# Kernel optimization log

Hardware: AMD Instinct MI355X
Metric: run time of the kernel (lower is better)

Reference implementation:

```python
import jax, jax.numpy as jnp
import numpy as np

EPS = 1e-5

def conv1x1(x, w, b):
    # x: [B,C,H,W], w: [O,C], b: [O]
    return jnp.einsum('bchw,oc->bohw', x, w) + b[None, :, None, None]

def bn(x, gamma, beta, mean, var):
    scale = gamma * jax.lax.rsqrt(var + EPS)
    return x * scale[None, :, None, None] + (beta - mean * scale)[None, :, None, None]

def setup_inputs() -> dict:
    key = jax.random.key(0)
    ks = jax.random.split(key, 20)
    B, C, H, W = 4, 64, 512, 512
    O = C
    d = {'feature': jax.random.normal(ks[0], (B, C, H, W), dtype=jnp.float32)}
    i = 1
    for name in ('q', 'k', 'v'):
        d[f'w_{name}'] = jax.random.normal(ks[i], (O, C), dtype=jnp.float32) * 0.05; i += 1
        d[f'b_{name}'] = jnp.zeros((O,), dtype=jnp.float32)
        d[f'gamma_{name}'] = jnp.ones((O,), dtype=jnp.float32)
        d[f'beta_{name}'] = jnp.zeros((O,), dtype=jnp.float32)
        d[f'mean_{name}'] = jax.random.normal(ks[i], (O,), dtype=jnp.float32) * 0.1; i += 1
        d[f'var_{name}'] = jax.random.uniform(ks[i], (O,), dtype=jnp.float32) + 0.5; i += 1
    d['w_out'] = jax.random.normal(ks[i], (O, O), dtype=jnp.float32) * 0.05; i += 1
    d['b_out'] = jnp.zeros((O,), dtype=jnp.float32)
    d['gamma_out'] = jnp.ones((O,), dtype=jnp.float32)
    d['beta_out'] = jnp.zeros((O,), dtype=jnp.float32)
    d['mean_out'] = jax.random.normal(ks[i], (O,), dtype=jnp.float32) * 0.1; i += 1
    d['var_out'] = jax.random.uniform(ks[i], (O,), dtype=jnp.float32) + 0.5
    return d

def reference(feature,
              w_q, b_q, gamma_q, beta_q, mean_q, var_q,
              w_k, b_k, gamma_k, beta_k, mean_k, var_k,
              w_v, b_v, gamma_v, beta_v, mean_v, var_v,
              w_out, b_out, gamma_out, beta_out, mean_out, var_out):
    # feature: [B,C,H,W]; attention treats H as sequence, W as feature dim per (b,c)
    q = bn(conv1x1(feature, w_q, b_q), gamma_q, beta_q, mean_q, var_q)
    k = bn(conv1x1(feature, w_k, b_k), gamma_k, beta_k, mean_k, var_k)
    v = bn(conv1x1(feature, w_v, b_v), gamma_v, beta_v, mean_v, var_v)
    W = q.shape[-1]
    scale = 1.0 / jnp.sqrt(jnp.float32(W))
    # scores: [B,C,H,H] = q @ k^T over the W axis
    scores = jnp.einsum('bchw,bcgw->bchg', q, k) * scale
    attn = jax.nn.softmax(scores, axis=-1)
    attn_out = jnp.einsum('bchg,bcgw->bchw', attn, v)  # [B,C,H,W]
    out = bn(conv1x1(attn_out, w_out, b_out), gamma_out, beta_out, mean_out, var_out)
    # dropout is identity in eval mode
    return out + feature
```

## Files before the change

### kernel.cpp

```cpp
#include <hip/hip_runtime.h>
#include <math.h>

typedef unsigned short u16;
typedef unsigned int u32;
typedef unsigned long long u64;
typedef __attribute__((ext_vector_type(8))) short bf16x8;
typedef __attribute__((ext_vector_type(4))) float f32x4;

#define MFMA16(a,b,c) __builtin_amdgcn_mfma_f32_16x16x32_bf16(a,b,c,0,0,0)

typedef __attribute__((address_space(1))) const unsigned int as1_u32;
typedef __attribute__((address_space(3))) unsigned int as3_u32;
__device__ __forceinline__ void gld16(const u16* g, u16* l){
  __builtin_amdgcn_global_load_lds((as1_u32*)g, (as3_u32*)l, 16, 0, 0);
}

__device__ __forceinline__ u16 f2bf(float x){
  union { float f; u32 u; } v; v.f = x;
  u32 u = v.u;
  return (u16)((u + 0x7fffu + ((u>>16)&1u)) >> 16);
}

__device__ __forceinline__ void memfence(){ asm volatile("" ::: "memory"); }

union B8 { bf16x8 v; u32 u[4]; uint4 q; };

__global__ void k0_prep(const float* wm, const float* bias, const float* gamma,
                        const float* beta, const float* mean, const float* var,
                        float extra, u16* wdst, float* ddst)
{
  int t = threadIdx.x;
  if (t < 64){
    float a0 = gamma[t] * rsqrtf(var[t] + 1e-5f);
    ddst[t] = (beta[t] + (bias[t] - mean[t]) * a0) * extra;
  }
  for (int i = t; i < 4096; i += 256){
    int o = i >> 6;
    float a0 = gamma[o] * rsqrtf(var[o] + 1e-5f);
    wdst[i] = f2bf(wm[i] * a0 * extra);
  }
}

__global__ __launch_bounds__(256,3)
void k1_qkv(const float* __restrict__ f, const u16* __restrict__ wz,
            const float* __restrict__ dz, u16* __restrict__ q,
            u16* __restrict__ kk_, u16* __restrict__ vt)
{
  int bid = blockIdx.x;
  int b  = bid >> 8;
  int ht = (bid >> 3) & 31;
  int wt = bid & 7;
  int tid = threadIdx.x;
  int wv = tid >> 6, lane = tid & 63;
  int l15 = lane & 15, l4 = lane >> 4;
  int h0 = ht * 16;
  int w0 = wt * 64 + wv * 16;

  bf16x8 wa[3][4][2];
  #pragma unroll
  for (int mt=0; mt<3; mt++)
    #pragma unroll
    for (int m=0;m<4;m++)
      #pragma unroll
      for (int ks=0;ks<2;ks++){
        B8 t; t.q = *(const uint4*)(wz + mt*4096 + (m*16+l15)*64 + ks*32 + l4*8);
        wa[mt][m][ks] = t.v;
      }
  f32x4 dv[3][4];
  #pragma unroll
  for (int mt=0;mt<3;mt++)
    #pragma unroll
    for (int m=0;m<4;m++)
      dv[mt][m] = *(const f32x4*)(dz + mt*64 + m*16 + l4*4);

  __shared__ u16 vstage[4][8704];
  u16* vs = vstage[wv];

  B8 bf[2];
  #pragma unroll
  for (int ks=0;ks<2;ks++)
    #pragma unroll
    for (int jj=0;jj<4;jj++){
      int c0 = ks*32 + l4*8 + jj*2;
      size_t i0 = ((size_t)(b*64 + c0)*512 + h0)*512 + w0 + l15;
      bf[ks].u[jj] = (u32)f2bf(f[i0]) | ((u32)f2bf(f[i0 + 262144]) << 16);
    }

  for (int hh=0; hh<16; hh++){
    int h = h0 + hh;
    B8 bfn[2];
    if (hh < 15){
      #pragma unroll
      for (int ks=0;ks<2;ks++)
        #pragma unroll
        for (int jj=0;jj<4;jj++){
          int c0 = ks*32 + l4*8 + jj*2;
          size_t i0 = ((size_t)(b*64 + c0)*512 + h + 1)*512 + w0 + l15;
          bfn[ks].u[jj] = (u32)f2bf(f[i0]) | ((u32)f2bf(f[i0 + 262144]) << 16);
        }
    }
    #pragma unroll
    for (int mt=0; mt<3; mt++){
      f32x4 acc[4];
      #pragma unroll
      for (int m=0;m<4;m++) acc[m] = (f32x4){0.f,0.f,0.f,0.f};
      #pragma unroll
      for (int m=0;m<4;m++)
        #pragma unroll
        for (int ks=0;ks<2;ks++)
          acc[m] = MFMA16(wa[mt][m][ks], bf[ks].v, acc[m]);
      #pragma unroll
      for (int m=0;m<4;m++)
        #pragma unroll
        for (int r=0;r<4;r++){
          float val = acc[m][r] + dv[mt][m][r];
          u16 bv = f2bf(val);
          int o = m*16 + l4*4 + r;
          if (mt==0)      q  [((size_t)(b*64+o)*512 + h)*512 + w0 + l15] = bv;
          else if (mt==1) kk_[((size_t)(b*64+o)*512 + h)*512 + w0 + l15] = bv;
          else            vs[o*136 + l15*8 + (hh&7)] = bv;
        }
    }
    bf[0] = bfn[0]; bf[1] = bfn[1];
    if ((hh&7)==7){
      __syncthreads();
      int hbg = (h - 7) >> 3;
      #pragma unroll
      for (int rr=0; rr<16; rr++){
        int o = rr*4 + l4;
        uint4 d = *(const uint4*)(vs + o*136 + l15*8);
        *(uint4*)(vt + (size_t)(b*64+o)*262144 + (size_t)hbg*4096
                     + (size_t)(w0+l15)*8) = d;
      }
      __syncthreads();
    }
  }
}

__global__ __launch_bounds__(512,2)
void k23_attn(const u16* __restrict__ q, const u16* __restrict__ kten,
              const u16* __restrict__ vt, u16* __restrict__ o2)
{
  int phys = blockIdx.x;
  int x = phys & 7, j = phys >> 3;
  int qt = j & 3, hh = j >> 2;
  int head = x*32 + hh;
  int q0 = qt*128;
  int b = head >> 6, c = head & 63;

  int tid = threadIdx.x;
  int wv = tid >> 6, lane = tid & 63;
  int l15 = lane & 15, l4 = lane >> 4;

  const u16* qh = q    + (size_t)head*262144;
  const u16* kh = kten + (size_t)head*262144;
  const u16* vh = vt   + (size_t)head*262144;

  __shared__ u16 KB[2][16640];
  __shared__ u16 VB[16384];
  __shared__ u16 Pt[5120];

  auto stageK = [&](int jt, int buf){
    const u16* src = kh + (size_t)jt*16384;
    #pragma unroll
    for (int i=0;i<4;i++){
      int row = i*8 + wv;
      gld16(src + (size_t)row*512 + lane*8, &KB[buf][row*520 + lane*8]);
    }
  };
  auto stageV = [&](int jt){
    const u16* src = vh + (size_t)jt*16384;
    #pragma unroll
    for (int i=0;i<4;i++){
      int slot = i*512 + tid;
      int w = slot >> 2, cc = slot & 3;
      int hbl = (cc - (w>>1)) & 3;
      gld16(src + hbl*4096 + w*8, &VB[slot*8]);
    }
  };

  uint4 qreg[16];
  {
    const u16* qrow = qh + (size_t)(q0 + wv*16 + l15)*512;
    #pragma unroll
    for (int ks=0;ks<16;ks++) qreg[ks] = *(const uint4*)(qrow + ks*32 + l4*8);
  }
  stageK(0, 0); stageV(0); stageK(1, 1);
  asm volatile("s_waitcnt vmcnt(4)" ::: "memory");
  __builtin_amdgcn_s_barrier(); memfence();

  f32x4 oacc[32];
  #pragma unroll
  for (int n=0;n<32;n++) oacc[n] = (f32x4){0.f,0.f,0.f,0.f};
  float m_run[4] = {-1e30f,-1e30f,-1e30f,-1e30f};
  float l_run[4] = {0.f,0.f,0.f,0.f};

  const int kbase = l15*520 + l4*8;
  const int vbase = l15*32  + (((l4 + (l15>>1)) & 3) << 3);
  const int pbase = (wv*16 + l15)*40;
  const int prow  = (wv*16 + l4*4)*40;

  for (int jt=0; jt<16; ++jt){
    int cur = jt & 1;
    const u16* Kc = &KB[cur][0];

    f32x4 sA[2], sB[2];
    #pragma unroll
    for (int n=0;n<2;n++){ sA[n]=(f32x4){0,0,0,0}; sB[n]=(f32x4){0,0,0,0}; }
    __builtin_amdgcn_s_setprio(1);
    #pragma unroll
    for (int ks=0; ks<8; ++ks){
      B8 a; a.q = qreg[ks];
      #pragma unroll
      for (int n=0;n<2;n++){
        B8 bb; bb.q = *(const uint4*)(Kc + kbase + n*8320 + ks*32);
        sA[n] = MFMA16(a.v, bb.v, sA[n]);
      }
    }
    #pragma unroll
    for (int ks=8; ks<16; ++ks){
      B8 a; a.q = qreg[ks];
      #pragma unroll
      for (int n=0;n<2;n++){
        B8 bb; bb.q = *(const uint4*)(Kc + kbase + n*8320 + ks*32);
        sB[n] = MFMA16(a.v, bb.v, sB[n]);
      }
    }
    __builtin_amdgcn_s_setprio(0);
    f32x4 sacc0 = sA[0] + sB[0];
    f32x4 sacc1 = sA[1] + sB[1];

    float pm[4], fc[4];
    bool need = false;
    #pragma unroll
    for (int r=0;r<4;r++){
      float p = fmaxf(sacc0[r], sacc1[r]);
      #pragma unroll
      for (int d=1; d<16; d<<=1) p = fmaxf(p, __shfl_xor(p, d, 64));
      pm[r] = p;
      need = need || (p > m_run[r] + 4.0f);
    }
    if (__any(need ? 1 : 0)){
      #pragma unroll
      for (int r=0;r<4;r++){
        float mn = fmaxf(m_run[r], pm[r]);
        fc[r] = exp2f(m_run[r] - mn);
        m_run[r] = mn;
      }
      #pragma unroll
      for (int n=0;n<32;n++)
        #pragma unroll
        for (int r=0;r<4;r++) oacc[n][r] *= fc[r];
    } else {
      fc[0]=fc[1]=fc[2]=fc[3]=1.0f;
    }
    #pragma unroll
    for (int r=0;r<4;r++){
      float e0 = exp2f(sacc0[r] - m_run[r]);
      float e1 = exp2f(sacc1[r] - m_run[r]);
      float s = e0 + e1;
      #pragma unroll
      for (int d=1; d<16; d<<=1) s += __shfl_xor(s, d, 64);
      l_run[r] = l_run[r]*fc[r] + s;
      Pt[prow + r*40 + l15]      = f2bf(e0);
      Pt[prow + r*40 + 16 + l15] = f2bf(e1);
    }

    asm volatile("s_waitcnt lgkmcnt(0)" ::: "memory");
    __builtin_amdgcn_s_barrier(); memfence();

    if (jt < 14) stageK(jt+2, cur);
    if (jt < 14)      { asm volatile("s_waitcnt vmcnt(4)" ::: "memory"); }
    else              { asm volatile("s_waitcnt vmcnt(0)" ::: "memory"); }
    __builtin_amdgcn_s_barrier(); memfence();

    B8 pa; pa.q = *(const uint4*)(Pt + pbase + l4*8);
    __builtin_amdgcn_s_setprio(1);
    #pragma unroll
    for (int n=0;n<32;n++){
      B8 bb; bb.q = *(const uint4*)(VB + vbase + n*512);
      oacc[n] = MFMA16(pa.v, bb.v, oacc[n]);
    }
    __builtin_amdgcn_s_setprio(0);

    if (jt < 15){
      asm volatile("s_waitcnt lgkmcnt(0)" ::: "memory");
      __builtin_amdgcn_s_barrier(); memfence();
      stageV(jt+1);
    }
  }

  u16* dst = o2 + (size_t)b*33554432 + 16777216
                + (size_t)(c>>1)*524288 + (c&1);
  #pragma unroll
  for (int r=0;r<4;r++){
    float inv = 1.0f / l_run[r];
    int qq = q0 + wv*16 + l4*4 + r;
    #pragma unroll
    for (int n=0;n<32;n++){
      int w = n*16 + l15;
      dst[(size_t)qq*1024 + w*2] = f2bf(oacc[n][r]*inv);
    }
  }
}

__global__ __launch_bounds__(512,2)
void k4_out(const u16* __restrict__ o2, const u16* __restrict__ wz,
            const float* __restrict__ dz, const float* __restrict__ f,
            float* __restrict__ out)
{
  int bid = blockIdx.x;
  int b = bid >> 9;
  int h = bid & 511;
  int tid = threadIdx.x, wv = tid>>6, lane = tid&63;
  int l15 = lane&15, l4 = lane>>4;

  __shared__ u16 Ost[32*1032];

  const u16* src0 = o2 + (size_t)b*33554432 + 16777216 + (size_t)h*1024;
  #pragma unroll
  for (int jj=0;jj<4;jj++){
    int row = jj*8 + wv;
    const u16* srow = src0 + (size_t)row*524288;
    #pragma unroll
    for (int hf=0;hf<2;hf++){
      gld16(srow + hf*512 + lane*8, &Ost[row*1032 + hf*512 + lane*8]);
    }
  }

  bf16x8 wa[4][2];
  #pragma unroll
  for (int m=0;m<4;m++)
    #pragma unroll
    for (int ks=0;ks<2;ks++){
      B8 t; t.q = *(const uint4*)(wz + 3*4096 + (m*16+l15)*64 + ks*32 + l4*8);
      wa[m][ks] = t.v;
    }
  f32x4 dvv[4];
  #pragma unroll
  for (int m=0;m<4;m++) dvv[m] = *(const f32x4*)(dz + 3*64 + m*16 + l4*4);

  asm volatile("s_waitcnt vmcnt(0)" ::: "memory");
  __syncthreads();

  f32x4 acc[4][4];
  #pragma unroll
  for (int m=0;m<4;m++)
    #pragma unroll
    for (int n=0;n<4;n++) acc[m][n] = (f32x4){0.f,0.f,0.f,0.f};

  const u16* obase = Ost + l4*4128 + wv*128 + l15*2;
  #pragma unroll
  for (int ks=0;ks<2;ks++){
    #pragma unroll
    for (int n=0;n<4;n++){
      B8 bb;
      #pragma unroll
      for (int jj=0;jj<4;jj++)
        bb.u[jj] = *(const u32*)(obase + ks*16512 + jj*1032 + n*32);
      #pragma unroll
      for (int m=0;m<4;m++)
        acc[m][n] = MFMA16(wa[m][ks], bb.v, acc[m][n]);
    }
  }
  #pragma unroll
  for (int m=0;m<4;m++)
    #pragma unroll
    for (int n=0;n<4;n++)
      #pragma unroll
      for (int r=0;r<4;r++){
        int o = m*16 + l4*4 + r;
        int w = wv*64 + n*16 + l15;
        size_t idx = ((size_t)(b*64+o)*512 + h)*512 + w;
        out[idx] = acc[m][n][r] + dvv[m][r] + f[idx];
      }
}

extern "C" void kernel_launch(void* const* d_in, const int* in_sizes, int n_in,
                              void* d_out, int out_size, void* d_ws, size_t ws_size,
                              hipStream_t stream) {
  const float* feat = (const float*)d_in[0];
  char* ws = (char*)d_ws;
  u16*   wz   = (u16*)ws;
  float* dz   = (float*)(ws + 32768);
  u16* bufQ = (u16*)(ws + 65536);
  u16* bufK = bufQ + 67108864ull;
  u16* bufV = bufK + 67108864ull;
  u16* o2   = (u16*)d_out;

  float extraK = 1.4426950408889634f / sqrtf(512.0f);
  for (int m=0; m<4; m++){
    int base = 1 + m*6;
    float extra = (m==1) ? extraK : 1.0f;
    k0_prep<<<dim3(1), dim3(256), 0, stream>>>(
        (const float*)d_in[base+0], (const float*)d_in[base+1],
        (const float*)d_in[base+2], (const float*)d_in[base+3],
        (const float*)d_in[base+4], (const float*)d_in[base+5],
        extra, wz + m*4096, dz + m*64);
  }
  k1_qkv   <<<dim3(1024), dim3(256), 0, stream>>>(feat, wz, dz, bufQ, bufK, bufV);
  k23_attn <<<dim3(1024), dim3(512), 0, stream>>>(bufQ, bufK, bufV, o2);
  k4_out   <<<dim3(2048), dim3(512), 0, stream>>>(o2, wz, dz, feat, (float*)d_out);
}
```

Before: 622.0 us.

## Process 64-key tiles per attention iteration and merge prep launches

The attention loop now handles 64 keys per iteration instead of 32, giving 8 iterations with twice the MFMA work per softmax and barrier round. K is no longer double-buffered; K and V halves are staged as 64-row tiles, and the four score accumulators are combined in one max/exp pass. This removes half of the barriers and online-softmax rescale checks, but K prefetch overlaps less with compute. The four single-block weight-prep launches are also merged into one 4-block launch to cut launch overhead.

```diff
diff --git a/kernel.cpp b/kernel.cpp
--- a/kernel.cpp
+++ b/kernel.cpp
@@ -25,10 +25,23 @@
 
 union B8 { bf16x8 v; u32 u[4]; uint4 q; };
 
-__global__ void k0_prep(const float* wm, const float* bias, const float* gamma,
-                        const float* beta, const float* mean, const float* var,
-                        float extra, u16* wdst, float* ddst)
+__global__ void k0_prep4(
+    const float* w0,const float* b0,const float* g0,const float* e0,const float* m0,const float* v0,
+    const float* w1,const float* b1,const float* g1,const float* e1,const float* m1,const float* v1,
+    const float* w2,const float* b2,const float* g2,const float* e2,const float* m2,const float* v2,
+    const float* w3,const float* b3,const float* g3,const float* e3,const float* m3,const float* v3,
+    float extraK, u16* wz, float* dz)
 {
+  int m = blockIdx.x;
+  const float* W[4]={w0,w1,w2,w3}; const float* B[4]={b0,b1,b2,b3};
+  const float* G[4]={g0,g1,g2,g3}; const float* E[4]={e0,e1,e2,e3};
+  const float* M[4]={m0,m1,m2,m3}; const float* V[4]={v0,v1,v2,v3};
+  const float* wm=W[m]; const float* bias=B[m]; const float* gamma=G[m];
+  const float* beta=E[m]; const float* mean=M[m]; const float* var=V[m];
+  float extra = (m==1) ? extraK : 1.0f;
+  u16* wdst = wz + m*4096;
+  float* ddst = dz + m*64;
+
   int t = threadIdx.x;
   if (t < 64){
     float a0 = gamma[t] * rsqrtf(var[t] + 1e-5f);
@@ -156,26 +169,32 @@
   const u16* kh = kten + (size_t)head*262144;
   const u16* vh = vt   + (size_t)head*262144;
 
-  __shared__ u16 KB[2][16640];
-  __shared__ u16 VB[16384];
-  __shared__ u16 Pt[5120];
-
-  auto stageK = [&](int jt, int buf){
-    const u16* src = kh + (size_t)jt*16384;
-    #pragma unroll
-    for (int i=0;i<4;i++){
-      int row = i*8 + wv;
-      gld16(src + (size_t)row*512 + lane*8, &KB[buf][row*520 + lane*8]);
+  __shared__ u16 KH[2][16640];
+  __shared__ u16 VH[2][16384];
+  __shared__ u16 PH[2][5120];
+
+  auto stageK64 = [&](int jt){
+    #pragma unroll
+    for (int h=0;h<2;h++){
+      const u16* src = kh + (size_t)jt*32768 + h*16384;
+      #pragma unroll
+      for (int i=0;i<4;i++){
+        int row = i*8 + wv;
+        gld16(src + (size_t)row*512 + lane*8, &KH[h][row*520 + lane*8]);
+      }
     }
   };
-  auto stageV = [&](int jt){
-    const u16* src = vh + (size_t)jt*16384;
-    #pragma unroll
-    for (int i=0;i<4;i++){
-      int slot = i*512 + tid;
-      int w = slot >> 2, cc = slot & 3;
-      int hbl = (cc - (w>>1)) & 3;
-      gld16(src + hbl*4096 + w*8, &VB[slot*8]);
+  auto stageV64 = [&](int jt){
+    #pragma unroll
+    for (int h=0;h<2;h++){
+      const u16* src = vh + (size_t)jt*32768 + h*16384;
+      #pragma unroll
+      for (int i=0;i<4;i++){
+        int slot = i*512 + tid;
+        int w = slot >> 2, cc = slot & 3;
+        int hbl = (cc - (w>>1)) & 3;
+        gld16(src + hbl*4096 + w*8, &VH[h][slot*8]);
+      }
     }
   };
 
@@ -185,8 +204,8 @@
     #pragma unroll
     for (int ks=0;ks<16;ks++) qreg[ks] = *(const uint4*)(qrow + ks*32 + l4*8);
   }
-  stageK(0, 0); stageV(0); stageK(1, 1);
-  asm volatile("s_waitcnt vmcnt(4)" ::: "memory");
+  stageK64(0); stageV64(0);
+  asm volatile("s_waitcnt vmcnt(0)" ::: "memory");
   __builtin_amdgcn_s_barrier(); memfence();
 
   f32x4 oacc[32];
@@ -200,41 +219,34 @@
   const int pbase = (wv*16 + l15)*40;
   const int prow  = (wv*16 + l4*4)*40;
 
-  for (int jt=0; jt<16; ++jt){
-    int cur = jt & 1;
-    const u16* Kc = &KB[cur][0];
-
-    f32x4 sA[2], sB[2];
-    #pragma unroll
-    for (int n=0;n<2;n++){ sA[n]=(f32x4){0,0,0,0}; sB[n]=(f32x4){0,0,0,0}; }
+  for (int jt=0; jt<8; ++jt){
+    if (jt > 0){
+      asm volatile("s_waitcnt vmcnt(8)" ::: "memory");
+      __builtin_amdgcn_s_barrier(); memfence();
+    }
+
+    f32x4 s0={0.f,0.f,0.f,0.f}, s1={0.f,0.f,0.f,0.f};
+    f32x4 s2={0.f,0.f,0.f,0.f}, s3={0.f,0.f,0.f,0.f};
     __builtin_amdgcn_s_setprio(1);
     #pragma unroll
-    for (int ks=0; ks<8; ++ks){
+    for (int ks=0; ks<16; ++ks){
       B8 a; a.q = qreg[ks];
-      #pragma unroll
-      for (int n=0;n<2;n++){
-        B8 bb; bb.q = *(const uint4*)(Kc + kbase + n*8320 + ks*32);
-        sA[n] = MFMA16(a.v, bb.v, sA[n]);
-      }
-    }
-    #pragma unroll
-    for (int ks=8; ks<16; ++ks){
-      B8 a; a.q = qreg[ks];
-      #pragma unroll
-      for (int n=0;n<2;n++){
-        B8 bb; bb.q = *(const uint4*)(Kc + kbase + n*8320 + ks*32);
-        sB[n] = MFMA16(a.v, bb.v, sB[n]);
-      }
+      B8 b0; b0.q = *(const uint4*)(&KH[0][0] + kbase + 0*8320 + ks*32);
+      B8 b1; b1.q = *(const uint4*)(&KH[0][0] + kbase + 1*8320 + ks*32);
+      B8 b2; b2.q = *(const uint4*)(&KH[1][0] + kbase + 0*8320 + ks*32);
+      B8 b3; b3.q = *(const uint4*)(&KH[1][0] + kbase + 1*8320 + ks*32);
+      s0 = MFMA16(a.v, b0.v, s0);
+      s1 = MFMA16(a.v, b1.v, s1);
+      s2 = MFMA16(a.v, b2.v, s2);
+      s3 = MFMA16(a.v, b3.v, s3);
     }
     __builtin_amdgcn_s_setprio(0);
-    f32x4 sacc0 = sA[0] + sB[0];
-    f32x4 sacc1 = sA[1] + sB[1];
 
     float pm[4], fc[4];
     bool need = false;
     #pragma unroll
     for (int r=0;r<4;r++){
-      float p = fmaxf(sacc0[r], sacc1[r]);
+      float p = fmaxf(fmaxf(s0[r], s1[r]), fmaxf(s2[r], s3[r]));
       #pragma unroll
       for (int d=1; d<16; d<<=1) p = fmaxf(p, __shfl_xor(p, d, 64));
       pm[r] = p;
@@ -256,37 +268,44 @@
     }
     #pragma unroll
     for (int r=0;r<4;r++){
-      float e0 = exp2f(sacc0[r] - m_run[r]);
-      float e1 = exp2f(sacc1[r] - m_run[r]);
-      float s = e0 + e1;
+      float e0 = exp2f(s0[r] - m_run[r]);
+      float e1 = exp2f(s1[r] - m_run[r]);
+      float e2 = exp2f(s2[r] - m_run[r]);
+      float e3 = exp2f(s3[r] - m_run[r]);
+      float s = (e0+e1)+(e2+e3);
       #pragma unroll
       for (int d=1; d<16; d<<=1) s += __shfl_xor(s, d, 64);
       l_run[r] = l_run[r]*fc[r] + s;
-      Pt[prow + r*40 + l15]      = f2bf(e0);
-      Pt[prow + r*40 + 16 + l15] = f2bf(e1);
+      PH[0][prow + r*40 + l15]      = f2bf(e0);
+      PH[0][prow + r*40 + 16 + l15] = f2bf(e1);
+      PH[1][prow + r*40 + l15]      = f2bf(e2);
+      PH[1][prow + r*40 + 16 + l15] = f2bf(e3);
     }
 
     asm volatile("s_waitcnt lgkmcnt(0)" ::: "memory");
     __builtin_amdgcn_s_barrier(); memfence();
 
-    if (jt < 14) stageK(jt+2, cur);
-    if (jt < 14)      { asm volatile("s_waitcnt vmcnt(4)" ::: "memory"); }
-    else              { asm volatile("s_waitcnt vmcnt(0)" ::: "memory"); }
+    if (jt < 7) stageK64(jt+1);
+    if (jt < 7) { asm volatile("s_waitcnt vmcnt(8)" ::: "memory"); }
+    else        { asm volatile("s_waitcnt vmcnt(0)" ::: "memory"); }
     __builtin_amdgcn_s_barrier(); memfence();
 
-    B8 pa; pa.q = *(const uint4*)(Pt + pbase + l4*8);
+    B8 paA; paA.q = *(const uint4*)(&PH[0][0] + pbase + l4*8);
+    B8 paB; paB.q = *(const uint4*)(&PH[1][0] + pbase + l4*8);
     __builtin_amdgcn_s_setprio(1);
     #pragma unroll
     for (int n=0;n<32;n++){
-      B8 bb; bb.q = *(const uint4*)(VB + vbase + n*512);
-      oacc[n] = MFMA16(pa.v, bb.v, oacc[n]);
+      B8 b0; b0.q = *(const uint4*)(&VH[0][0] + vbase + n*512);
+      B8 b1; b1.q = *(const uint4*)(&VH[1][0] + vbase + n*512);
+      oacc[n] = MFMA16(paA.v, b0.v, oacc[n]);
+      oacc[n] = MFMA16(paB.v, b1.v, oacc[n]);
     }
     __builtin_amdgcn_s_setprio(0);
 
-    if (jt < 15){
+    if (jt < 7){
       asm volatile("s_waitcnt lgkmcnt(0)" ::: "memory");
       __builtin_amdgcn_s_barrier(); memfence();
-      stageV(jt+1);
+      stageV64(jt+1);
     }
   }
 
@@ -389,15 +408,16 @@
   u16* o2   = (u16*)d_out;
 
   float extraK = 1.4426950408889634f / sqrtf(512.0f);
-  for (int m=0; m<4; m++){
-    int base = 1 + m*6;
-    float extra = (m==1) ? extraK : 1.0f;
-    k0_prep<<<dim3(1), dim3(256), 0, stream>>>(
-        (const float*)d_in[base+0], (const float*)d_in[base+1],
-        (const float*)d_in[base+2], (const float*)d_in[base+3],
-        (const float*)d_in[base+4], (const float*)d_in[base+5],
-        extra, wz + m*4096, dz + m*64);
-  }
+  k0_prep4<<<dim3(4), dim3(256), 0, stream>>>(
+      (const float*)d_in[1],  (const float*)d_in[2],  (const float*)d_in[3],
+      (const float*)d_in[4],  (const float*)d_in[5],  (const float*)d_in[6],
+      (const float*)d_in[7],  (const float*)d_in[8],  (const float*)d_in[9],
+      (const float*)d_in[10], (const float*)d_in[11], (const float*)d_in[12],
+      (const float*)d_in[13], (const float*)d_in[14], (const float*)d_in[15],
+      (const float*)d_in[16], (const float*)d_in[17], (const float*)d_in[18],
+      (const float*)d_in[19], (const float*)d_in[20], (const float*)d_in[21],
+      (const float*)d_in[22], (const float*)d_in[23], (const float*)d_in[24],
+      extraK, wz, dz);
   k1_qkv   <<<dim3(1024), dim3(256), 0, stream>>>(feat, wz, dz, bufQ, bufK, bufV);
   k23_attn <<<dim3(1024), dim3(512), 0, stream>>>(bufQ, bufK, bufV, o2);
   k4_out   <<<dim3(2048), dim3(512), 0, stream>>>(o2, wz, dz, feat, (float*)d_out);
```

After: 650.5 us. +4.6%, slower.
